# Kernel tuning notes

Measured on AMD Instinct MI355X. Metric: run time of the kernel, lower is better.

## Reference

```python
import jax, jax.numpy as jnp
import numpy as np
from itertools import product

N_CODONS = 2
ORDER = 2
N_STATES = 25          # calc_number_of_states() with nCodons=2
ALPHA6 = 6             # alphabet_size + 2
OFFSET = 8 + 3 * N_CODONS       # 14, first insert state
TERM1 = OFFSET + 3 * (N_CODONS + 1)  # 23, terminal_1 state

CODE = {'A': [0], 'C': [1], 'G': [2], 'T': [3], 'N': [0, 1, 2, 3], 'X': [5]}


def _state_entries(state, emissions, x_must_preceed):
    ems = ['N'] * (ORDER - len(emissions) + 1) + list(emissions)[-(ORDER + 1):]
    allowed = [[state]]
    for i, e in enumerate(ems):
        allowed.append(CODE[e] + ([4] if i < ORDER - x_must_preceed else []))
    out = []
    for x in product(*allowed):
        found, ok = False, True
        for i in range(1, ORDER + 1):
            if found and x[i] == 4:
                ok = False
                break
            if x[i] != 4:
                found = True
        if ok:
            out.append(x)
    return out


def _emission_index_spec():
    entries, k = [], 0
    def add(state, ems, xp, trainable=True):
        nonlocal k
        ids = _state_entries(state, ems, xp)
        for t, x in enumerate(ids):
            entries.append((x, k + t if trainable else -1))
        if trainable:
            k += len(ids)
    add(0, 'N', 0); add(1, 'A', 0); add(2, 'AT', 0); add(3, 'ATG', 0, False)
    add(4, 'ATGN', 0); add(5, 'ATGNN', 0)
    for s in range(6, 6 + N_CODONS * 3 - 2):
        add(s, 'N', 0)
    add(4 + 3 * N_CODONS, 'T', ORDER)
    add(5 + 3 * N_CODONS, 'TA', ORDER); add(5 + 3 * N_CODONS, 'TG', ORDER)
    add(6 + 3 * N_CODONS, 'TAA', ORDER, False)
    add(6 + 3 * N_CODONS, 'TAG', ORDER, False)
    add(6 + 3 * N_CODONS, 'TGA', ORDER, False)
    add(7 + 3 * N_CODONS, 'N', ORDER)
    for s in range(8 + 3 * N_CODONS, 8 + 3 * N_CODONS + 3 * (N_CODONS + 1)):
        add(s, 'N', 0)
    for i in range(1, ORDER + 1):
        add(TERM1, 'X' * i, ORDER)
    add(TERM1 + 1, 'X' * (ORDER + 1), ORDER, False)
    idx = np.array([e[0] for e in entries], dtype=np.int32)
    widx = np.array([e[1] for e in entries], dtype=np.int32)
    return idx, widx

EM_IDX, EM_WIDX = _emission_index_spec()


def build_A(w):
    # sparse transition structure -> row-softmax over nonzeros -> dense [25,25]
    idx, vals = [], []
    def add(i, j, v):
        idx.append((i, j)); vals.append(v)
    n, k = N_CODONS, 0
    add(0, 0, 1 - w[k]); add(0, 1, w[k]); k += 1
    add(1, 2, 1.0); add(2, 3, 1.0)
    for i in range(n):
        add(3 + 3 * i, 4 + 3 * i, w[k + i])
    k += n
    for i in range(n):
        add(4 + 3 * i, 5 + 3 * i, 1.0)
    for i in range(n):
        add(5 + 3 * i, 6 + 3 * i, 1.0)
    for i in range(n + 1):
        add(3 + 3 * i, OFFSET + 3 * i, w[k + i])
    k += n + 1
    add(3 + 3 * n, 4 + 3 * n, 1 - w[k - 1])
    for i in range(n + 1):
        add(OFFSET + 3 * i, OFFSET + 1 + 3 * i, 1.0)
    for i in range(n + 1):
        add(OFFSET + 1 + 3 * i, OFFSET + 2 + 3 * i, 1.0)
    for i in range(n + 1):
        add(OFFSET + 2 + 3 * i, 4 + 3 * i, w[k + i])
    for i in range(n + 1):
        add(OFFSET + 2 + 3 * i, OFFSET + 3 * i, 1 - w[k + i])
    k += n + 1
    i_del = [3 + 3 * i for i in range(n) for _ in range(n - i)]
    j_del = [4 + 3 * j for i in range(1, n + 1) for j in range(i, n + 1)]
    for i, j in zip(i_del, j_del):
        add(i, j, 1 - w[k] * w[k] ** ((j - i) // 3))
    k += 1
    add(4 + 3 * n, 5 + 3 * n, 1.0); add(5 + 3 * n, 6 + 3 * n, 1.0)
    add(6 + 3 * n, 7 + 3 * n, 1.0)
    add(7 + 3 * n, 7 + 3 * n, 1.0); add(7 + 3 * n, TERM1, 1.0)
    add(TERM1, TERM1, 1.0); add(TERM1, TERM1 + 1, 1.0)
    add(TERM1 + 1, TERM1 + 1, 1.0)
    rows = np.array([i for i, _ in idx]); cols = np.array([j for _, j in idx])
    logits = jnp.stack([jnp.asarray(v, jnp.float32) for v in vals])
    M = jnp.full((N_STATES, N_STATES), -jnp.inf, jnp.float32).at[rows, cols].set(logits)
    A = jax.nn.softmax(M, axis=-1)
    return jnp.where(jnp.isfinite(M), A, 0.0)


def build_B(w):
    # sparse emission values (trainable weights or fixed 1), per-state softmax over nonzeros
    vals = jnp.where(EM_WIDX >= 0, w[np.clip(EM_WIDX, 0, None)], 1.0)
    rows = EM_IDX[:, 0]
    flat = EM_IDX[:, 1] * 36 + EM_IDX[:, 2] * 6 + EM_IDX[:, 3]
    M = jnp.full((N_STATES, ALPHA6 ** 3), -jnp.inf, jnp.float32).at[rows, flat].set(vals)
    B = jax.nn.softmax(M, axis=-1)
    return jnp.where(jnp.isfinite(M), B, 0.0)  # [25, 216]


def build_I(w):
    n_init = 3 + 3 * N_CODONS  # states 0..8 get initial mass
    p = jax.nn.softmax(w[:n_init])
    return jnp.zeros((N_STATES,), jnp.float32).at[:n_init].set(p)


def _forward(transition_kernel, emission_kernel, init_kernel, tokens):
    A = build_A(transition_kernel)
    Bf = build_B(emission_kernel)
    I = build_I(init_kernel)
    Bt, T = tokens.shape
    pad = jnp.full((Bt, ORDER), 4, tokens.dtype)  # '4' = no preceding emission
    tp = jnp.concatenate([pad, tokens], axis=1)
    flat = tp[:, :-2] * 36 + tp[:, 1:-1] * 6 + tp[:, 2:]  # [Bt, T]
    E = jnp.moveaxis(Bf.T[flat], 1, 0)  # [T, Bt, 25]
    alpha = I[None, :] * E[0]
    s = alpha.sum(-1, keepdims=True)
    alpha = alpha / s
    ll = jnp.log(s[..., 0])
    def step(carry, e):
        a, ll = carry
        a = (a @ A) * e
        s = a.sum(-1, keepdims=True)
        return (a / s, ll + jnp.log(s[..., 0])), None
    (alpha, ll), _ = jax.lax.scan(step, (alpha, ll), E[1:])
    return ll  # [Bt] per-sequence log-likelihood


def setup_inputs() -> dict:
    key = jax.random.key(0)
    k1, k2, k3, k4 = jax.random.split(key, 4)
    return {
        'transition_kernel': jax.random.normal(k1, (10,), jnp.float32) * 0.05,
        'emission_kernel': jax.random.normal(k2, (5400,), jnp.float32) * 0.05,
        'init_kernel': jax.random.normal(k3, (25,), jnp.float32) * 0.05,
        'tokens': jax.random.randint(k4, (512, 2048), 0, 4, jnp.int32),
    }


def reference(transition_kernel, emission_kernel, init_kernel, tokens):
    return _forward(transition_kernel, emission_kernel, init_kernel, tokens)
```

## Files before the change

kernel.cpp:

```cpp
#include <hip/hip_runtime.h>
#include <hip/hip_bf16.h>
#include <math.h>


typedef float v2f __attribute__((ext_vector_type(2)));
typedef float v4f __attribute__((ext_vector_type(4)));

#define NSTATES 25
#define NLIVE   23
#define NFLAT   216
#define NPACK   100
#define TLEN    2048
#define NSEQ    512
#define CHUNKS  16
#define CLEN    128

#define LOG16 2.772588722239781f

__device__ __constant__ int PERMC[24] = {1,4,2,5,3,6,7,10,8,11,9,12,
                                         14,17,15,18,16,19,20,0,21,13,22,23};
__device__ __constant__ int POSA[NLIVE] = {19,0,2,4,1,3,5,6,8,10,7,9,11,21,
                                           12,14,16,13,15,17,18,20,22};

__device__ __align__(16) float gBt[NPACK * 32];

struct WMap { short m[NSTATES * NFLAT]; };

constexpr WMap make_wmap() {
  WMap w{};
  for (int i = 0; i < NSTATES * NFLAT; i++) w.m[i] = -2;
  const unsigned char ST[29] = {0,1,2,3,4,5,6,7,8,9,10,11,11,12,12,12,13,
                                14,15,16,17,18,19,20,21,22,23,23,24};
  const unsigned char M1[29] = {0x1F,0x1F,0x1F,0x11,0x18,0x14,0x1F,0x1F,0x1F,
                                0x1F,0x0F,0x0F,0x0F,0x08,0x08,0x08,0x0F,
                                0x1F,0x1F,0x1F,0x1F,0x1F,0x1F,0x1F,0x1F,0x1F,
                                0x0F,0x0F,0x20};
  const unsigned char M2[29] = {0x1F,0x1F,0x11,0x18,0x14,0x1F,0x1F,0x1F,0x1F,
                                0x1F,0x0F,0x08,0x08,0x01,0x01,0x04,0x0F,
                                0x1F,0x1F,0x1F,0x1F,0x1F,0x1F,0x1F,0x1F,0x1F,
                                0x0F,0x20,0x20};
  const unsigned char M3[29] = {0x0F,0x01,0x08,0x04,0x0F,0x0F,0x0F,0x0F,0x0F,
                                0x0F,0x08,0x01,0x04,0x01,0x04,0x01,0x0F,
                                0x0F,0x0F,0x0F,0x0F,0x0F,0x0F,0x0F,0x0F,0x0F,
                                0x20,0x20,0x20};
  const unsigned char TR[29] = {1,1,1,0,1,1,1,1,1,1,1,1,1,0,0,0,1,
                                1,1,1,1,1,1,1,1,1,1,1,0};
  int k = 0;
  for (int s = 0; s < 29; s++) {
    for (int c1 = 0; c1 < 6; c1++) {
      if (!((M1[s] >> c1) & 1)) continue;
      for (int c2 = 0; c2 < 6; c2++) {
        if (!((M2[s] >> c2) & 1)) continue;
        if (c1 != 4 && c2 == 4) continue;
        for (int c3 = 0; c3 < 6; c3++) {
          if (!((M3[s] >> c3) & 1)) continue;
          w.m[ST[s] * NFLAT + c1 * 36 + c2 * 6 + c3] =
              TR[s] ? (short)(k++) : (short)-1;
        }
      }
    }
  }
  return w;
}
__device__ __constant__ WMap WMAP = make_wmap();

__device__ __forceinline__ unsigned short f2bf(float x) {
  unsigned int u = __float_as_uint(x);
  u += 0x7fffu + ((u >> 16) & 1u);
  return (unsigned short)(u >> 16);
}

struct Wp {
  v2f w01, wA, wB, wC, wD, wE, wF;
  float w4, w5, w8, w11;
};

__device__ __forceinline__ void step_pk(v2f (&Q)[12], const v4f (&F)[6],
                                        const Wp& W) {
  float a0 = Q[9].y,  a3 = Q[2].x,  a6 = Q[2].y,  a9 = Q[5].x;
  float a12 = Q[5].y, a13 = Q[10].y, a16 = Q[8].x, a19 = Q[8].y, a22 = Q[11].x;
  float q9x = Q[9].x, q10x = Q[10].x;

  v2f t01 = a0 * W.w01;
  v2f t44 = a3 * W.wA + a16 * W.wB;
  v2f t77 = a6 * W.wC + a19 * W.wD;
  float n7  = fmaf(a3, W.w4, t77.x);
  v2f tAA = a9 * W.wE + a22 * W.wF;
  float n10 = fmaf(a3, W.w5, fmaf(a6, W.w8, tAA.x));
  float n13 = fmaf(a13, W.w11, a12);

  v2f nQ1 = Q[0] * __builtin_shufflevector(F[0], F[0], 2, 3);
  v2f nQ2 = Q[1] * __builtin_shufflevector(F[1], F[1], 0, 1);
  v2f nQ4 = Q[3] * __builtin_shufflevector(F[2], F[2], 0, 1);
  v2f nQ5 = Q[4] * __builtin_shufflevector(F[2], F[2], 2, 3);
  v2f nQ7 = Q[6] * __builtin_shufflevector(F[3], F[3], 2, 3);
  v2f nQ8 = Q[7] * __builtin_shufflevector(F[4], F[4], 0, 1);

  Q[0]  = (v2f){ t01.y * F[0].x, t44.x * F[0].y };
  Q[3]  = (v2f){ n7    * F[1].z, n10   * F[1].w };
  Q[6]  = (v2f){ t44.y * F[3].x, t77.y * F[3].y };
  Q[9]  = (v2f){ tAA.y * F[4].z, t01.x * F[4].w };
  Q[10] = (v2f){ q9x   * F[5].x, n13   * F[5].y };
  Q[11].x = q10x * F[5].z;
  Q[1] = nQ1; Q[2] = nQ2; Q[4] = nQ4; Q[5] = nQ5; Q[7] = nQ7; Q[8] = nQ8;
}

__device__ __forceinline__ void renorm_pk(v2f (&Q)[12], float& L) {
  v2f acc = ((Q[0] + Q[1]) + (Q[2] + Q[3])) + ((Q[4] + Q[5]) + (Q[6] + Q[7]))
          + ((Q[8] + Q[9]) + (Q[10] + Q[11]));
  float s = acc.x + acc.y;
  if (s > 0.0f) {
    L += __logf(s);
    float r = __fdividef(1.0f, s);
    #pragma unroll
    for (int k = 0; k < 12; k++) Q[k] *= r;
  } else {
    L = -3.0e38f;
  }
}

#define LDROW(F, nt_) { int nt = (nt_); \
  const int roff = ((c12 << 2) + nt) << 5; \
  const v4f* er = (const v4f*)(sBt + roff); \
  const v4f* gr = (const v4f*)(gBt + roff); \
  F[0] = er[0]; F[1] = er[1]; F[2] = er[2]; \
  F[3] = gr[3]; F[4] = gr[4]; F[5] = gr[5]; \
  c12 = p2 * 5 + nt; p2 = nt; }
#define LDSTEP(Fn, Fc, nt_) { LDROW(Fn, nt_); step_pk(Q, Fc, W); }

__global__ __launch_bounds__(32)
void prep_kernel(const float* __restrict__ wE) {
  const int st  = blockIdx.x;
  const int row = threadIdx.x;
  const int pos = POSA[st];
  float part = 0.0f;
  for (int c = row; c < NFLAT; c += 32) {
    short m = WMAP.m[st * NFLAT + c];
    if (m == -1) part += expf(1.0f);
    else if (m >= 0) part += expf(wE[m]);
  }
  #pragma unroll
  for (int m = 1; m < 32; m <<= 1) part += __shfl_xor(part, m, 32);
  float inv = 16.0f / part;
  for (int i = row; i < NPACK; i += 32) {
    int c12 = i >> 2, nt = i & 3;
    int p1 = c12 / 5, p2v = c12 - 5 * p1;
    int flat = p1 * 36 + p2v * 6 + nt;
    short m = WMAP.m[st * NFLAT + flat];
    float v = 0.0f;
    if (m == -1) v = expf(1.0f);
    else if (m >= 0) v = expf(wE[m]);
    gBt[i * 32 + pos] = v * inv;
  }
  if (st == 0) {
    for (int i = row; i < NPACK; i += 32) gBt[i * 32 + 23] = 0.0f;
  }
}

__global__ __launch_bounds__(512)
void hmm_kernel(const float* __restrict__ wT, const float* __restrict__ wE,
                const float* __restrict__ wI, const int* __restrict__ tokens,
                float* __restrict__ out) {
  __shared__ __align__(16) float          sBt[NPACK * 32];
  __shared__ __align__(16) unsigned short sT[CHUNKS * NLIVE * 24];
  __shared__ float sL[CHUNKS * NLIVE];
  __shared__ float sAW[24];
  __shared__ float sI[32];

  const int tid   = threadIdx.x;
  const int seq   = blockIdx.x;
  const int chunk = tid >> 5;
  const int row   = tid & 31;
  const int* trow = tokens + (size_t)seq * TLEN;

  for (int st = chunk; st < NLIVE; st += 16) {
    const int pos = POSA[st];
    float part = 0.0f;
    for (int c = row; c < NFLAT; c += 32) {
      short m = WMAP.m[st * NFLAT + c];
      if (m == -1) part += expf(1.0f);
      else if (m >= 0) part += expf(wE[m]);
    }
    #pragma unroll
    for (int m = 1; m < 32; m <<= 1) part += __shfl_xor(part, m, 32);
    float inv = 16.0f / part;
    for (int i = row; i < NPACK; i += 32) {
      int c12 = i >> 2, nt = i & 3;
      int p1 = c12 / 5, p2v = c12 - 5 * p1;
      int flat = p1 * 36 + p2v * 6 + nt;
      short m = WMAP.m[st * NFLAT + flat];
      float v = 0.0f;
      if (m == -1) v = expf(1.0f);
      else if (m >= 0) v = expf(wE[m]);
      sBt[i * 32 + pos] = v * inv;
    }
  }
  for (int i = tid; i < NPACK; i += 512) sBt[i * 32 + 23] = 0.0f;
  if (tid == 480) {
    const float w0 = wT[0], w1 = wT[1], w2 = wT[2], w3 = wT[3], w4 = wT[4];
    const float w5 = wT[5], w6 = wT[6], w7 = wT[7], w8 = wT[8], w9 = wT[9];
    { float e0 = expf(1.0f - w0), e1 = expf(w0), is = 1.0f / (e0 + e1);
      sAW[0] = e0 * is; sAW[1] = e1 * is; }
    { float e4 = expf(w1), e14 = expf(w3);
      float e7 = expf(1.0f - w9 * w9), e10 = expf(1.0f - w9 * w9 * w9);
      float is = 1.0f / (e4 + e14 + e7 + e10);
      sAW[2] = e4 * is;  sAW[3] = e14 * is;
      sAW[4] = e7 * is;  sAW[5] = e10 * is; }
    { float e7 = expf(w2), e17 = expf(w4), e10 = expf(1.0f - w9 * w9);
      float is = 1.0f / (e7 + e17 + e10);
      sAW[6] = e7 * is; sAW[7] = e17 * is; sAW[8] = e10 * is; }
    { float e20 = expf(w5), e10 = expf(1.0f - w5), is = 1.0f / (e20 + e10);
      sAW[9] = e20 * is; sAW[10] = e10 * is; }
    sAW[11] = 0.5f; sAW[12] = 0.5f;
    { float e4 = expf(w6), e14 = expf(1.0f - w6), is = 1.0f / (e4 + e14);
      sAW[13] = e4 * is; sAW[14] = e14 * is; }
    { float e7 = expf(w7), e17 = expf(1.0f - w7), is = 1.0f / (e7 + e17);
      sAW[15] = e7 * is; sAW[16] = e17 * is; }
    { float e10 = expf(w8), e20 = expf(1.0f - w8), is = 1.0f / (e10 + e20);
      sAW[17] = e10 * is; sAW[18] = e20 * is; }
    sAW[19] = 0.5f; sAW[20] = 0.5f;
  } else if (tid == 481) {
    float e[9], s = 0.0f;
    for (int i = 0; i < 9; i++) { e[i] = expf(wI[i]); s += e[i]; }
    float inv = 1.0f / s;
    for (int i = 0; i < 9; i++) sI[i] = e[i] * inv;
    for (int i = 9; i < 32; i++) sI[i] = 0.0f;
  }
  __syncthreads();

  float w[21];
  #pragma unroll
  for (int i = 0; i < 21; i++)
    w[i] = __uint_as_float(
        (unsigned)__builtin_amdgcn_readfirstlane(__float_as_uint(sAW[i])));
  Wp W;
  W.w01 = (v2f){w[0],  w[1]};
  W.wA  = (v2f){w[2],  w[3]};
  W.wB  = (v2f){w[13], w[14]};
  W.wC  = (v2f){w[6],  w[7]};
  W.wD  = (v2f){w[15], w[16]};
  W.wE  = (v2f){w[10], w[9]};
  W.wF  = (v2f){w[17], w[18]};
  W.w4 = w[4]; W.w5 = w[5]; W.w8 = w[8]; W.w11 = w[11];

  const int t0 = chunk * CLEN;

  v2f Q[12];
  #pragma unroll
  for (int k = 0; k < 12; k++) {
    Q[k].x = (row == PERMC[2 * k]) ? 1.0f : 0.0f;
    Q[k].y = (row == PERMC[2 * k + 1]) ? 1.0f : 0.0f;
  }
  float L = 0.0f;

  v4f FA[6], FB[6];
  int c12, p2;
  int4 q0 = *(const int4*)(trow + t0);
  int4 q1 = *(const int4*)(trow + t0 + 4);

  int b = 0;
  if (chunk == 0) {
    c12 = 20 + q0.x; p2 = q0.x;
    LDROW(FA, q0.y);
    LDSTEP(FB, FA, q0.z);
    LDSTEP(FA, FB, q0.w);
    LDSTEP(FB, FA, q1.x);
    LDSTEP(FA, FB, q1.y);
    LDSTEP(FB, FA, q1.z);
    LDSTEP(FA, FB, q1.w);
    step_pk(Q, FA, W);
    b = 1;
    q0 = *(const int4*)(trow + 8);
    q1 = *(const int4*)(trow + 12);
  } else {
    int2 pp = *(const int2*)(trow + t0 - 2);
    c12 = pp.x * 5 + pp.y; p2 = pp.y;
  }

  for (; b < CLEN / 8; b++) {
    int4 n0 = q0, n1 = q1;
    if (b + 1 < CLEN / 8) {
      n0 = *(const int4*)(trow + t0 + (b + 1) * 8);
      n1 = *(const int4*)(trow + t0 + (b + 1) * 8 + 4);
    }
    LDROW(FA, q0.x);
    LDSTEP(FB, FA, q0.y);
    LDSTEP(FA, FB, q0.z);
    LDSTEP(FB, FA, q0.w);
    LDSTEP(FA, FB, q1.x);
    LDSTEP(FB, FA, q1.y);
    LDSTEP(FA, FB, q1.z);
    LDSTEP(FB, FA, q1.w);
    step_pk(Q, FB, W);
    if (b & 1) renorm_pk(Q, L);
    q0 = n0; q1 = n1;
  }

  if (L > -1.0e38f) L -= (chunk == 0 ? 127.0f : 128.0f) * LOG16;

  if (row < NLIVE) {
    const int base = (chunk * NLIVE + row) * 24;
    #pragma unroll
    for (int k = 0; k < 12; k++) {
      ushort2 p; p.x = f2bf(Q[k].x); p.y = f2bf(Q[k].y);
      *(ushort2*)&sT[base + 2 * k] = p;
    }
    sL[chunk * NLIVE + row] = L;
  }
  __syncthreads();

  if (tid < 64) {
    const int lane = tid;
    const bool act = (lane < NLIVE);

    int jp = 23;
    #pragma unroll
    for (int pos = 0; pos < 23; pos++)
      if (PERMC[pos] == lane) jp = pos;

    const int tok0 = trow[0];
    const int idx0 = 96 + tok0;

    float v = act ? sI[lane] * sBt[idx0 * 32 + jp] : 0.0f;
    float s = v;
    #pragma unroll
    for (int m = 1; m < 32; m <<= 1) s += __shfl_xor(s, m, 32);
    float ll = __logf(s) - LOG16;
    v = act ? v * __fdividef(1.0f, s) : 0.0f;

    for (int c = 0; c < CHUNKS; c++) {
      float Lj  = act ? sL[c * NLIVE + lane] : -3.0e38f;
      float key = (act && v > 0.0f) ? Lj : -3.0e38f;
      float mx = key;
      #pragma unroll
      for (int m = 1; m < 32; m <<= 1) mx = fmaxf(mx, __shfl_xor(mx, m, 32));
      float wgt = (act && v > 0.0f) ? v * __expf(Lj - mx) : 0.0f;

      float nv = 0.0f;
      #pragma unroll
      for (int r = 0; r < NLIVE; r++) {
        float wr = __shfl(wgt, r, 64);
        nv += wr * __uint_as_float(((unsigned)sT[(c * NLIVE + r) * 24 + jp]) << 16);
      }
      float nva = act ? nv : 0.0f;
      float s2 = nva;
      #pragma unroll
      for (int m = 1; m < 32; m <<= 1) s2 += __shfl_xor(s2, m, 32);
      ll += mx + __logf(s2);
      v = act ? nv * __fdividef(1.0f, s2) : 0.0f;
    }

    if (lane == 0) out[seq] = ll;
  }
}

extern "C" void kernel_launch(void* const* d_in, const int* in_sizes, int n_in,
                              void* d_out, int out_size, void* d_ws, size_t ws_size,
                              hipStream_t stream) {
  const float* wT = (const float*)d_in[0];
  const float* wE = (const float*)d_in[1];
  const float* wI = (const float*)d_in[2];
  const int* tokens = (const int*)d_in[3];
  float* out = (float*)d_out;
  (void)d_ws; (void)ws_size;

  prep_kernel<<<NLIVE, 32, 0, stream>>>(wE);
  hmm_kernel<<<NSEQ, 512, 0, stream>>>(wT, wE, wI, tokens, out);
}
```

Measured before the change: 139.6 us.

## Prefetch global emission rows two steps ahead and move more columns to LDS

The emission row for each step is split differently: four v4f now come from shared memory instead of three, and only two come from global memory. The global part is fetched two steps ahead through a four-slot rotating register ring, with its address computed directly from token triples. This is meant to hide global/L2 latency on the serial recurrence's critical path, at the cost of more registers and more LDS bandwidth per step.

```diff
diff --git a/kernel.cpp b/kernel.cpp
--- a/kernel.cpp
+++ b/kernel.cpp
@@ -75,8 +75,8 @@
   float w4, w5, w8, w11;
 };
 
-__device__ __forceinline__ void step_pk(v2f (&Q)[12], const v4f (&F)[6],
-                                        const Wp& W) {
+__device__ __forceinline__ void step_pk(v2f (&Q)[12], const v4f (&D)[4],
+                                        const v4f (&G)[2], const Wp& W) {
   float a0 = Q[9].y,  a3 = Q[2].x,  a6 = Q[2].y,  a9 = Q[5].x;
   float a12 = Q[5].y, a13 = Q[10].y, a16 = Q[8].x, a19 = Q[8].y, a22 = Q[11].x;
   float q9x = Q[9].x, q10x = Q[10].x;
@@ -89,19 +89,19 @@
   float n10 = fmaf(a3, W.w5, fmaf(a6, W.w8, tAA.x));
   float n13 = fmaf(a13, W.w11, a12);
 
-  v2f nQ1 = Q[0] * __builtin_shufflevector(F[0], F[0], 2, 3);
-  v2f nQ2 = Q[1] * __builtin_shufflevector(F[1], F[1], 0, 1);
-  v2f nQ4 = Q[3] * __builtin_shufflevector(F[2], F[2], 0, 1);
-  v2f nQ5 = Q[4] * __builtin_shufflevector(F[2], F[2], 2, 3);
-  v2f nQ7 = Q[6] * __builtin_shufflevector(F[3], F[3], 2, 3);
-  v2f nQ8 = Q[7] * __builtin_shufflevector(F[4], F[4], 0, 1);
-
-  Q[0]  = (v2f){ t01.y * F[0].x, t44.x * F[0].y };
-  Q[3]  = (v2f){ n7    * F[1].z, n10   * F[1].w };
-  Q[6]  = (v2f){ t44.y * F[3].x, t77.y * F[3].y };
-  Q[9]  = (v2f){ tAA.y * F[4].z, t01.x * F[4].w };
-  Q[10] = (v2f){ q9x   * F[5].x, n13   * F[5].y };
-  Q[11].x = q10x * F[5].z;
+  v2f nQ1 = Q[0] * __builtin_shufflevector(D[0], D[0], 2, 3);
+  v2f nQ2 = Q[1] * __builtin_shufflevector(D[1], D[1], 0, 1);
+  v2f nQ4 = Q[3] * __builtin_shufflevector(D[2], D[2], 0, 1);
+  v2f nQ5 = Q[4] * __builtin_shufflevector(D[2], D[2], 2, 3);
+  v2f nQ7 = Q[6] * __builtin_shufflevector(D[3], D[3], 2, 3);
+  v2f nQ8 = Q[7] * __builtin_shufflevector(G[0], G[0], 0, 1);
+
+  Q[0]  = (v2f){ t01.y * D[0].x, t44.x * D[0].y };
+  Q[3]  = (v2f){ n7    * D[1].z, n10   * D[1].w };
+  Q[6]  = (v2f){ t44.y * D[3].x, t77.y * D[3].y };
+  Q[9]  = (v2f){ tAA.y * G[0].z, t01.x * G[0].w };
+  Q[10] = (v2f){ q9x   * G[1].x, n13   * G[1].y };
+  Q[11].x = q10x * G[1].z;
   Q[1] = nQ1; Q[2] = nQ2; Q[4] = nQ4; Q[5] = nQ5; Q[7] = nQ7; Q[8] = nQ8;
 }
 
@@ -119,14 +119,14 @@
   }
 }
 
-#define LDROW(F, nt_) { int nt = (nt_); \
-  const int roff = ((c12 << 2) + nt) << 5; \
-  const v4f* er = (const v4f*)(sBt + roff); \
-  const v4f* gr = (const v4f*)(gBt + roff); \
-  F[0] = er[0]; F[1] = er[1]; F[2] = er[2]; \
-  F[3] = gr[3]; F[4] = gr[4]; F[5] = gr[5]; \
+#define LDROW_DS(D, nt_) { int nt = (nt_); \
+  const v4f* er = (const v4f*)(sBt + (((c12 << 2) + nt) << 5)); \
+  D[0] = er[0]; D[1] = er[1]; D[2] = er[2]; D[3] = er[3]; \
   c12 = p2 * 5 + nt; p2 = nt; }
-#define LDSTEP(Fn, Fc, nt_) { LDROW(Fn, nt_); step_pk(Q, Fc, W); }
+
+#define GLOAD(Gb, a_, b_, c_) { \
+  const v4f* gr = (const v4f*)(gBt + ((((a_) * 5 + (b_)) * 4 + (c_)) << 5)); \
+  Gb[0] = gr[4]; Gb[1] = gr[5]; }
 
 __global__ __launch_bounds__(32)
 void prep_kernel(const float* __restrict__ wE) {
@@ -253,7 +253,8 @@
   }
   float L = 0.0f;
 
-  v4f FA[6], FB[6];
+  v4f DA[4], DB[4];
+  v4f G0[2], G1[2], G2[2], G3[2];
   int c12, p2;
   int4 q0 = *(const int4*)(trow + t0);
   int4 q1 = *(const int4*)(trow + t0 + 4);
@@ -261,20 +262,32 @@
   int b = 0;
   if (chunk == 0) {
     c12 = 20 + q0.x; p2 = q0.x;
-    LDROW(FA, q0.y);
-    LDSTEP(FB, FA, q0.z);
-    LDSTEP(FA, FB, q0.w);
-    LDSTEP(FB, FA, q1.x);
-    LDSTEP(FA, FB, q1.y);
-    LDSTEP(FB, FA, q1.z);
-    LDSTEP(FA, FB, q1.w);
-    step_pk(Q, FA, W);
+    int4 nq0 = *(const int4*)(trow + 8);
+    int4 nq1 = *(const int4*)(trow + 12);
+    GLOAD(G0, 4, q0.x, q0.y);
+    GLOAD(G1, q0.x, q0.y, q0.z);
+    LDROW_DS(DA, q0.y);
+    GLOAD(G2, q0.y, q0.z, q0.w);
+    { LDROW_DS(DB, q0.z); step_pk(Q, DA, G0, W); }
+    GLOAD(G3, q0.z, q0.w, q1.x);
+    { LDROW_DS(DA, q0.w); step_pk(Q, DB, G1, W); }
+    GLOAD(G0, q0.w, q1.x, q1.y);
+    { LDROW_DS(DB, q1.x); step_pk(Q, DA, G2, W); }
+    GLOAD(G1, q1.x, q1.y, q1.z);
+    { LDROW_DS(DA, q1.y); step_pk(Q, DB, G3, W); }
+    GLOAD(G2, q1.y, q1.z, q1.w);
+    { LDROW_DS(DB, q1.z); step_pk(Q, DA, G0, W); }
+    GLOAD(G0, q1.z, q1.w, nq0.x);
+    { LDROW_DS(DA, q1.w); step_pk(Q, DB, G1, W); }
+    GLOAD(G1, q1.w, nq0.x, nq0.y);
+    step_pk(Q, DA, G2, W);
     b = 1;
-    q0 = *(const int4*)(trow + 8);
-    q1 = *(const int4*)(trow + 12);
+    q0 = nq0; q1 = nq1;
   } else {
     int2 pp = *(const int2*)(trow + t0 - 2);
     c12 = pp.x * 5 + pp.y; p2 = pp.y;
+    GLOAD(G0, pp.x, pp.y, q0.x);
+    GLOAD(G1, pp.y, q0.x, q0.y);
   }
 
   for (; b < CLEN / 8; b++) {
@@ -283,15 +296,23 @@
       n0 = *(const int4*)(trow + t0 + (b + 1) * 8);
       n1 = *(const int4*)(trow + t0 + (b + 1) * 8 + 4);
     }
-    LDROW(FA, q0.x);
-    LDSTEP(FB, FA, q0.y);
-    LDSTEP(FA, FB, q0.z);
-    LDSTEP(FB, FA, q0.w);
-    LDSTEP(FA, FB, q1.x);
-    LDSTEP(FB, FA, q1.y);
-    LDSTEP(FA, FB, q1.z);
-    LDSTEP(FB, FA, q1.w);
-    step_pk(Q, FB, W);
+    LDROW_DS(DA, q0.x);
+    GLOAD(G2, q0.x, q0.y, q0.z);
+    { LDROW_DS(DB, q0.y); step_pk(Q, DA, G0, W); }
+    GLOAD(G3, q0.y, q0.z, q0.w);
+    { LDROW_DS(DA, q0.z); step_pk(Q, DB, G1, W); }
+    GLOAD(G0, q0.z, q0.w, q1.x);
+    { LDROW_DS(DB, q0.w); step_pk(Q, DA, G2, W); }
+    GLOAD(G1, q0.w, q1.x, q1.y);
+    { LDROW_DS(DA, q1.x); step_pk(Q, DB, G3, W); }
+    GLOAD(G2, q1.x, q1.y, q1.z);
+    { LDROW_DS(DB, q1.y); step_pk(Q, DA, G0, W); }
+    GLOAD(G3, q1.y, q1.z, q1.w);
+    { LDROW_DS(DA, q1.z); step_pk(Q, DB, G1, W); }
+    GLOAD(G0, q1.z, q1.w, n0.x);
+    { LDROW_DS(DB, q1.w); step_pk(Q, DA, G2, W); }
+    GLOAD(G1, q1.w, n0.x, n0.y);
+    step_pk(Q, DB, G3, W);
     if (b & 1) renorm_pk(Q, L);
     q0 = n0; q1 = n1;
   }
```

Measured after the change: 131.9 us. -5.5%, faster.
